# Performance work log

Measured on AMD Instinct MI355X. Metric: run time of the kernel, lower is better.

Reference implementation:

```python
import jax, jax.numpy as jnp
import numpy as np

VOCAB = 1024
PRED_H = 320
ENC_H = 1024
JOINT_H = 640


def setup_inputs() -> dict:
    key = jax.random.key(0)
    k_f, k_g, k_w1, k_b1, k_w2, k_b2 = jax.random.split(key, 6)
    B, T, U = 8, 256, 65
    f = jax.random.normal(k_f, (B, T, ENC_H), dtype=jnp.float32)
    g = jax.random.normal(k_g, (B, U, PRED_H), dtype=jnp.float32)
    in_dim = PRED_H + ENC_H
    s1 = 1.0 / np.sqrt(in_dim)
    s2 = 1.0 / np.sqrt(JOINT_H)
    # W1 acts on cat([f, g], axis=-1): rows [0:ENC_H] hit f, rows [ENC_H:] hit g
    W1 = jax.random.uniform(k_w1, (in_dim, JOINT_H), minval=-s1, maxval=s1, dtype=jnp.float32)
    b1 = jax.random.uniform(k_b1, (JOINT_H,), minval=-s1, maxval=s1, dtype=jnp.float32)
    W2 = jax.random.uniform(k_w2, (JOINT_H, VOCAB), minval=-s2, maxval=s2, dtype=jnp.float32)
    b2 = jax.random.uniform(k_b2, (VOCAB,), minval=-s2, maxval=s2, dtype=jnp.float32)
    return {"f": f, "g": g, "W1": W1, "b1": b1, "W2": W2, "b2": b2}


def reference(f, g, W1, b1, W2, b2):
    # Linear(cat(f_expand, g_expand)) == f @ W1[:ENC_H] + g @ W1[ENC_H:] + b1,
    # broadcast-added over (T, U). Same math as the torch module (dropout p=0 / eval).
    W1f = W1[:ENC_H]          # (ENC_H, JOINT_H)
    W1g = W1[ENC_H:]          # (PRED_H, JOINT_H)
    hf = jnp.einsum("bth,hj->btj", f, W1f)            # (B, T, J)
    hg = jnp.einsum("buh,hj->buj", g, W1g)            # (B, U, J)
    h = jax.nn.relu(hf[:, :, None, :] + hg[:, None, :, :] + b1)  # (B, T, U, J)
    logits = jnp.einsum("btuj,jk->btuk", h, W2) + b2  # (B, T, U, VOCAB)
    return logits
```

## Files before the change

kernel.cpp:

```cpp
#include <hip/hip_runtime.h>
#include <cstdint>

typedef __bf16 bf16;
typedef __bf16 bf16x8 __attribute__((ext_vector_type(8)));
typedef float  f32x4  __attribute__((ext_vector_type(4)));

__global__ __launch_bounds__(256) void gemm_small(
    const float* __restrict__ A, const float* __restrict__ Bm,
    const float* __restrict__ bias, bf16* __restrict__ Cout,
    int M, int N, int K)
{
    __shared__ float As[64][20];
    __shared__ float Bs[16][68];
    const int tid = threadIdx.x;
    const int m0 = blockIdx.x * 64, n0 = blockIdx.y * 64;
    const int tx = tid & 15, ty = tid >> 4;
    const int arow = tid >> 2, ak = (tid & 3) << 2;
    const int bk = tid >> 4, bc = (tid & 15) << 2;
    const bool avalid = (m0 + arow) < M;
    float acc[4][4] = {};

    for (int k0 = 0; k0 < K; k0 += 16) {
        float4 av = make_float4(0.f, 0.f, 0.f, 0.f);
        if (avalid) av = *(const float4*)&A[(size_t)(m0 + arow) * K + k0 + ak];
        float4 bv = *(const float4*)&Bm[(size_t)(k0 + bk) * N + n0 + bc];
        __syncthreads();
        *(float4*)&As[arow][ak] = av;
        *(float4*)&Bs[bk][bc] = bv;
        __syncthreads();
#pragma unroll
        for (int k = 0; k < 16; ++k) {
            float a[4], b[4];
#pragma unroll
            for (int i = 0; i < 4; ++i) a[i] = As[ty * 4 + i][k];
#pragma unroll
            for (int j = 0; j < 4; ++j) b[j] = Bs[k][tx * 4 + j];
#pragma unroll
            for (int i = 0; i < 4; ++i)
#pragma unroll
                for (int j = 0; j < 4; ++j) acc[i][j] += a[i] * b[j];
        }
    }
#pragma unroll
    for (int i = 0; i < 4; ++i) {
        int row = m0 + ty * 4 + i;
        if (row >= M) continue;
#pragma unroll
        for (int j = 0; j < 4; ++j) {
            int col = n0 + tx * 4 + j;
            float v = acc[i][j] + (bias ? bias[col] : 0.f);
            Cout[(size_t)row * N + col] = (bf16)v;
        }
    }
}

__global__ __launch_bounds__(256) void w2_transpose(
    const float* __restrict__ W2, bf16* __restrict__ W2T)
{
    __shared__ float t[32][33];
    const int tx = threadIdx.x, ty = threadIdx.y;
    const int n0 = blockIdx.x * 32, k0 = blockIdx.y * 32;
#pragma unroll
    for (int i = 0; i < 4; ++i)
        t[ty + i * 8][tx] = W2[(size_t)(k0 + ty + i * 8) * 1024 + n0 + tx];
    __syncthreads();
#pragma unroll
    for (int i = 0; i < 4; ++i)
        W2T[(size_t)(n0 + ty + i * 8) * 640 + k0 + tx] = (bf16)t[tx][ty + i * 8];
}

__global__ __launch_bounds__(512, 2) void joint_main(
    const bf16* __restrict__ hf, const bf16* __restrict__ hgb,
    const bf16* __restrict__ W2T, const float* __restrict__ b2,
    float* __restrict__ out)
{
    __shared__ bf16 As[2][256 * 64];
    __shared__ bf16 Bs[2][256 * 64];
    const int tid = threadIdx.x;
    const int n0 = blockIdx.x * 256;
    const int m0 = blockIdx.y * 256;

    const int r  = tid >> 2;
    const int kq = (tid & 3) << 4;
    const int c0 = (tid & 3) << 1;
    const int aoff0 = r * 64 + (((c0    ) ^ (r & 7)) << 3);
    const int aoff1 = r * 64 + (((c0 + 1) ^ (r & 7)) << 3);

    const bf16* hfp[2];
    const bf16* hgp[2];
#pragma unroll
    for (int h = 0; h < 2; ++h) {
        int m = m0 + h * 128 + r;
        int bt = m / 65;
        int uu = m - bt * 65;
        int bb = bt >> 8;
        hfp[h] = hf  + (size_t)bt * 640 + kq;
        hgp[h] = hgb + (size_t)(bb * 65 + uu) * 640 + kq;
    }

    const int wid = tid >> 6, lane = tid & 63;
    const int wr = wid >> 2, wc = wid & 3;
    const int lg = lane >> 4, l15 = lane & 15;

    bf16x8 F0[2], F1[2], G0[2], G1[2];

    auto loadA = [&](int k0) {
#pragma unroll
        for (int h = 0; h < 2; ++h) {
            F0[h] = *(const bf16x8*)(hfp[h] + k0);
            F1[h] = *(const bf16x8*)(hfp[h] + k0 + 8);
            G0[h] = *(const bf16x8*)(hgp[h] + k0);
            G1[h] = *(const bf16x8*)(hgp[h] + k0 + 8);
        }
    };
    auto stageB = [&](int buf, int k0) {
        const char* w2b = (const char*)W2T + (size_t)k0 * 2;
#pragma unroll
        for (int call = 0; call < 4; ++call) {
            int chunk = call * 512 + tid;
            int brow = chunk >> 3, c = chunk & 7;
            const char* src = w2b + (size_t)(n0 + brow) * 1280
                                  + ((c ^ (brow & 7)) << 4);
            __builtin_amdgcn_global_load_lds(
                (const __attribute__((address_space(1))) uint32_t*)src,
                (__attribute__((address_space(3))) uint32_t*)&Bs[buf][chunk << 3],
                16, 0, 0);
        }
    };
    auto genA = [&](int buf) {
#pragma unroll
        for (int h = 0; h < 2; ++h) {
            bf16x8 O0, O1;
#pragma unroll
            for (int i = 0; i < 8; ++i) {
                float s = (float)F0[h][i] + (float)G0[h][i];
                O0[i] = (bf16)fmaxf(s, 0.f);
            }
#pragma unroll
            for (int i = 0; i < 8; ++i) {
                float s = (float)F1[h][i] + (float)G1[h][i];
                O1[i] = (bf16)fmaxf(s, 0.f);
            }
            *(bf16x8*)&As[buf][h * 128 * 64 + aoff0] = O0;
            *(bf16x8*)&As[buf][h * 128 * 64 + aoff1] = O1;
        }
    };

    f32x4 acc[8][4] = {};

    loadA(0);
    stageB(0, 0);
    genA(0);
    __syncthreads();

    for (int t = 0; t < 10; ++t) {
        const int cur = t & 1;
        if (t < 9) {
            loadA((t + 1) * 64);
            stageB(cur ^ 1, (t + 1) * 64);
        }
#pragma unroll
        for (int kk = 0; kk < 2; ++kk) {
            const int clog = (kk << 2) + lg;
            bf16x8 bfr[4];
#pragma unroll
            for (int ni = 0; ni < 4; ++ni) {
                int row = wc * 64 + ni * 16 + l15;
                bfr[ni] = *(const bf16x8*)&Bs[cur][row * 64 + ((clog ^ (row & 7)) << 3)];
            }
#pragma unroll
            for (int mi = 0; mi < 8; ++mi) {
                int row = wr * 128 + mi * 16 + l15;
                bf16x8 a = *(const bf16x8*)&As[cur][row * 64 + ((clog ^ (row & 7)) << 3)];
#pragma unroll
                for (int ni = 0; ni < 4; ++ni)
                    acc[mi][ni] = __builtin_amdgcn_mfma_f32_16x16x32_bf16(
                        a, bfr[ni], acc[mi][ni], 0, 0, 0);
            }
        }
        if (t < 9) genA(cur ^ 1);
        __syncthreads();
    }

    float bv[4];
#pragma unroll
    for (int ni = 0; ni < 4; ++ni) bv[ni] = b2[n0 + wc * 64 + ni * 16 + l15];
#pragma unroll
    for (int mi = 0; mi < 8; ++mi) {
#pragma unroll
        for (int ni = 0; ni < 4; ++ni) {
            int col = n0 + wc * 64 + ni * 16 + l15;
#pragma unroll
            for (int j = 0; j < 4; ++j) {
                int row = m0 + wr * 128 + mi * 16 + lg * 4 + j;
                out[(size_t)row * 1024 + col] = acc[mi][ni][j] + bv[ni];
            }
        }
    }
}

extern "C" void kernel_launch(void* const* d_in, const int* in_sizes, int n_in,
                              void* d_out, int out_size, void* d_ws, size_t ws_size,
                              hipStream_t stream)
{
    const float* f  = (const float*)d_in[0];
    const float* g  = (const float*)d_in[1];
    const float* W1 = (const float*)d_in[2];
    const float* b1 = (const float*)d_in[3];
    const float* W2 = (const float*)d_in[4];
    const float* b2 = (const float*)d_in[5];
    float* out = (float*)d_out;

    bf16* hf  = (bf16*)d_ws;
    bf16* hgb = hf + 2048 * 640;
    bf16* W2T = hgb + 520 * 640;

    gemm_small<<<dim3(32, 10), 256, 0, stream>>>(f, W1, nullptr, hf, 2048, 640, 1024);
    gemm_small<<<dim3(9, 10), 256, 0, stream>>>(g, W1 + 1024 * 640, b1, hgb, 520, 640, 320);
    w2_transpose<<<dim3(32, 20), dim3(32, 8), 0, stream>>>(W2, W2T);
    joint_main<<<dim3(4, 520), 512, 0, stream>>>(hf, hgb, W2T, b2, out);
}
```

Baseline: 389.5 us.

## Interleave LDS fragment loads, MFMA phases and global staging with explicit barriers

```diff
diff --git a/kernel.cpp b/kernel.cpp
--- a/kernel.cpp
+++ b/kernel.cpp
@@ -4,6 +4,12 @@
 typedef __bf16 bf16;
 typedef __bf16 bf16x8 __attribute__((ext_vector_type(8)));
 typedef float  f32x4  __attribute__((ext_vector_type(4)));
+
+#define BARRIER()    asm volatile("s_barrier" ::: "memory")
+#define WAIT_LGKM0() do { asm volatile("s_waitcnt lgkmcnt(0)" ::: "memory"); \
+                          __builtin_amdgcn_sched_barrier(0); } while (0)
+#define WAIT_VM(n)   do { asm volatile("s_waitcnt vmcnt(" #n ")" ::: "memory"); \
+                          __builtin_amdgcn_sched_barrier(0); } while (0)
 
 __global__ __launch_bounds__(256) void gemm_small(
     const float* __restrict__ A, const float* __restrict__ Bm,
@@ -103,6 +109,8 @@
     const int lg = lane >> 4, l15 = lane & 15;
 
     bf16x8 F0[2], F1[2], G0[2], G1[2];
+    bf16x8 afr[4], bfr[4];
+    f32x4 acc[8][4] = {};
 
     auto loadA = [&](int k0) {
 #pragma unroll
@@ -113,10 +121,10 @@
             G1[h] = *(const bf16x8*)(hgp[h] + k0 + 8);
         }
     };
-    auto stageB = [&](int buf, int k0) {
+    auto stageB2 = [&](int buf, int k0, int call0) {
         const char* w2b = (const char*)W2T + (size_t)k0 * 2;
 #pragma unroll
-        for (int call = 0; call < 4; ++call) {
+        for (int call = call0; call < call0 + 2; ++call) {
             int chunk = call * 512 + tid;
             int brow = chunk >> 3, c = chunk & 7;
             const char* src = w2b + (size_t)(n0 + brow) * 1280
@@ -146,41 +154,74 @@
         }
     };
 
-    f32x4 acc[8][4] = {};
+#define LDB(cur, KK)                                                          \
+    { const int clog = ((KK) << 2) + lg;                                      \
+      _Pragma("unroll")                                                       \
+      for (int ni = 0; ni < 4; ++ni) {                                        \
+          int row = wc * 64 + ni * 16 + l15;                                  \
+          bfr[ni] = *(const bf16x8*)&Bs[cur][row * 64 + ((clog ^ (row & 7)) << 3)]; \
+      } }
+
+#define LDA(cur, KK, MH)                                                      \
+    { const int clog = ((KK) << 2) + lg;                                      \
+      _Pragma("unroll")                                                       \
+      for (int i = 0; i < 4; ++i) {                                           \
+          int row = wr * 128 + ((MH) * 4 + i) * 16 + l15;                     \
+          afr[i] = *(const bf16x8*)&As[cur][row * 64 + ((clog ^ (row & 7)) << 3)]; \
+      } }
+
+#define MFMA16(MH)                                                            \
+    { __builtin_amdgcn_s_setprio(1);                                          \
+      _Pragma("unroll")                                                       \
+      for (int i = 0; i < 4; ++i)                                             \
+          _Pragma("unroll")                                                   \
+          for (int ni = 0; ni < 4; ++ni)                                      \
+              acc[(MH) * 4 + i][ni] = __builtin_amdgcn_mfma_f32_16x16x32_bf16(\
+                  afr[i], bfr[ni], acc[(MH) * 4 + i][ni], 0, 0, 0);           \
+      __builtin_amdgcn_s_setprio(0); }
 
     loadA(0);
-    stageB(0, 0);
+    stageB2(0, 0, 0);
+    stageB2(0, 0, 2);
+    WAIT_VM(4);
     genA(0);
-    __syncthreads();
+    WAIT_VM(0);
+    WAIT_LGKM0();
+    BARRIER();
 
     for (int t = 0; t < 10; ++t) {
-        const int cur = t & 1;
+        const int cur = t & 1, nxt = cur ^ 1;
+        const int kn = (t + 1) * 64;
+        if (t < 9) loadA(kn);
+        LDB(cur, 0); LDA(cur, 0, 0);
+        BARRIER(); WAIT_LGKM0();
+        MFMA16(0);
+        BARRIER();
+        if (t < 9) stageB2(nxt, kn, 0);
+        LDA(cur, 0, 1);
+        BARRIER(); WAIT_LGKM0();
+        MFMA16(1);
+        BARRIER();
+        if (t < 9) stageB2(nxt, kn, 2);
+        LDB(cur, 1); LDA(cur, 1, 0);
+        BARRIER(); WAIT_LGKM0();
+        MFMA16(0);
+        BARRIER();
+        LDA(cur, 1, 1);
+        BARRIER(); WAIT_LGKM0();
+        MFMA16(1);
         if (t < 9) {
-            loadA((t + 1) * 64);
-            stageB(cur ^ 1, (t + 1) * 64);
-        }
-#pragma unroll
-        for (int kk = 0; kk < 2; ++kk) {
-            const int clog = (kk << 2) + lg;
-            bf16x8 bfr[4];
-#pragma unroll
-            for (int ni = 0; ni < 4; ++ni) {
-                int row = wc * 64 + ni * 16 + l15;
-                bfr[ni] = *(const bf16x8*)&Bs[cur][row * 64 + ((clog ^ (row & 7)) << 3)];
-            }
-#pragma unroll
-            for (int mi = 0; mi < 8; ++mi) {
-                int row = wr * 128 + mi * 16 + l15;
-                bf16x8 a = *(const bf16x8*)&As[cur][row * 64 + ((clog ^ (row & 7)) << 3)];
-#pragma unroll
-                for (int ni = 0; ni < 4; ++ni)
-                    acc[mi][ni] = __builtin_amdgcn_mfma_f32_16x16x32_bf16(
-                        a, bfr[ni], acc[mi][ni], 0, 0, 0);
-            }
-        }
-        if (t < 9) genA(cur ^ 1);
-        __syncthreads();
-    }
+            WAIT_VM(4);
+            genA(nxt);
+        }
+        WAIT_VM(0);
+        WAIT_LGKM0();
+        BARRIER();
+    }
+
+#undef LDB
+#undef LDA
+#undef MFMA16
 
     float bv[4];
 #pragma unroll
```

New measurement: 452.5 us. +16.2%, slower.
